# Kernel optimization log

Hardware: AMD Instinct MI355X
Metric: run time of the kernel (lower is better)

Reference implementation:

```python
import jax, jax.numpy as jnp
import numpy as np

NUM_EXPERTS = 8
TOP_K = 2


def setup_inputs() -> dict:
    key = jax.random.key(0)
    ks = jax.random.split(key, 5)
    B, T, D, H, E = 8, 4096, 512, 1536, NUM_EXPERTS
    scale = 0.02
    x = jax.random.normal(ks[0], (B, T, D), dtype=jnp.float32)
    gate_w = jax.random.normal(ks[1], (E, D), dtype=jnp.float32) * scale
    w1 = jax.random.normal(ks[2], (E, H, D), dtype=jnp.float32) * scale
    w3 = jax.random.normal(ks[3], (E, H, D), dtype=jnp.float32) * scale
    w2 = jax.random.normal(ks[4], (E, D, H), dtype=jnp.float32) * scale
    return {"x": x, "gate_w": gate_w, "w1": w1, "w3": w3, "w2": w2}


def reference(x, gate_w, w1, w3, w2):
    B, T, D = x.shape
    E = gate_w.shape[0]
    xf = x.reshape(-1, D)                      # [N, D], N = B*T
    N = xf.shape[0]
    gate_logits = xf @ gate_w.T                # [N, E]
    weights, indices = jax.lax.top_k(gate_logits, TOP_K)   # [N, K]
    weights = jax.nn.softmax(weights, axis=-1)
    # combine[n, e] = sum_k weights[n, k] * (indices[n, k] == e)
    combine = jnp.zeros((N, E), dtype=xf.dtype).at[
        jnp.arange(N)[:, None], indices].add(weights)       # [N, E]
    out = jnp.zeros_like(xf)
    for e in range(E):  # small fixed expert count
        h = jax.nn.silu(xf @ w1[e].T) * (xf @ w3[e].T)      # [N, H]
        y = h @ w2[e].T                                     # [N, D]
        out = out + combine[:, e:e + 1] * y
    return out.reshape(B, T, D)
```

## Files before the change

kernel.cpp:

```cpp
#include <hip/hip_runtime.h>


#define N_TOK 32768
#define DIM   512
#define HID   1536
#define NE    8
#define MTS   256

typedef __attribute__((ext_vector_type(8))) short  short8;
typedef __attribute__((ext_vector_type(4))) float  floatx4;

#define MFMA(a,b,c) __builtin_amdgcn_mfma_f32_16x16x32_bf16(a,b,c,0,0,0)

__device__ __forceinline__ unsigned short f2bf(float f) {
  unsigned int u = __float_as_uint(f);
  u += 0x7fffu + ((u >> 16) & 1u);
  return (unsigned short)(u >> 16);
}
__device__ __forceinline__ unsigned pk2(float a, float b) {
  return (unsigned)f2bf(a) | ((unsigned)f2bf(b) << 16);
}
__device__ __forceinline__ void gl_lds16(const unsigned short* g, unsigned short* l) {
  __builtin_amdgcn_global_load_lds(
      (const __attribute__((address_space(1))) unsigned int*)g,
      (__attribute__((address_space(3))) unsigned int*)l, 16, 0, 0);
}

__global__ void __launch_bounds__(256) cvt_kernel(const float* __restrict__ src,
                                                  unsigned short* __restrict__ dst,
                                                  int n4) {
  int i = blockIdx.x * 256 + threadIdx.x;
  if (i >= n4) return;
  float4 v = ((const float4*)src)[i];
  uint2 o; o.x = pk2(v.x, v.y); o.y = pk2(v.z, v.w);
  ((uint2*)dst)[i] = o;
}

__global__ void __launch_bounds__(256) gate1_kernel(const float* __restrict__ x,
                                                    const float* __restrict__ gw,
                                                    unsigned short* __restrict__ xb,
                                                    unsigned* __restrict__ eidx,
                                                    float* __restrict__ wts) {
  int lane = threadIdx.x & 63;
  int wave = threadIdx.x >> 6;
  int t = blockIdx.x * 4 + wave;

  const float4* xp = (const float4*)(x + (size_t)t * DIM + lane * 8);
  float4 x0 = xp[0], x1 = xp[1];

  uint4 o; o.x = pk2(x0.x, x0.y); o.y = pk2(x0.z, x0.w);
  o.z = pk2(x1.x, x1.y); o.w = pk2(x1.z, x1.w);
  *(uint4*)(xb + (size_t)t * DIM + lane * 8) = o;

  double p[NE];
#pragma unroll
  for (int e = 0; e < NE; ++e) {
    const float4* gp = (const float4*)(gw + e * DIM + lane * 8);
    float4 g0 = gp[0], g1 = gp[1];
    p[e] = (double)x0.x * g0.x + (double)x0.y * g0.y + (double)x0.z * g0.z + (double)x0.w * g0.w
         + (double)x1.x * g1.x + (double)x1.y * g1.y + (double)x1.z * g1.z + (double)x1.w * g1.w;
  }
#pragma unroll
  for (int m = 1; m < 64; m <<= 1) {
#pragma unroll
    for (int e = 0; e < NE; ++e) p[e] += __shfl_xor(p[e], m);
  }
  if (lane == 0) {
    double m1 = -1e300, m2 = -1e300; int i1 = 0, i2 = 0;
#pragma unroll
    for (int e = 0; e < NE; ++e) {
      double v = p[e];
      if (v > m1) { m2 = m1; i2 = i1; m1 = v; i1 = e; }
      else if (v > m2) { m2 = v; i2 = e; }
    }
    float e2 = __expf((float)(m2 - m1));
    float wa = 1.f / (1.f + e2);
    eidx[t] = (unsigned)i1 | ((unsigned)i2 << 8);
    wts[t]  = wa;
  }
}

__global__ void __launch_bounds__(256) gate2_kernel(const unsigned* __restrict__ eidx,
                                                    const float* __restrict__ wts,
                                                    int* __restrict__ tokl,
                                                    float* __restrict__ wgtl,
                                                    int* __restrict__ cnt) {
  __shared__ unsigned hist[NE];
  __shared__ unsigned basep[NE];
  int tid = threadIdx.x;
  if (tid < NE) hist[tid] = 0;
  __syncthreads();
  int t0 = blockIdx.x * 1024;
  unsigned pk[4]; float wv[4];
#pragma unroll
  for (int i = 0; i < 4; ++i) {
    int t = t0 + tid + i * 256;
    pk[i] = eidx[t]; wv[i] = wts[t];
    atomicAdd(&hist[pk[i] & 0xff], 1u);
    atomicAdd(&hist[(pk[i] >> 8) & 0xff], 1u);
  }
  __syncthreads();
  if (tid < NE) {
    basep[tid] = (unsigned)atomicAdd(&cnt[tid], (int)hist[tid]);
    hist[tid] = 0;
  }
  __syncthreads();
#pragma unroll
  for (int i = 0; i < 4; ++i) {
    int t = t0 + tid + i * 256;
    int e1 = pk[i] & 0xff, e2 = (pk[i] >> 8) & 0xff;
    unsigned p1 = basep[e1] + atomicAdd(&hist[e1], 1u);
    tokl[e1 * N_TOK + p1] = t; wgtl[e1 * N_TOK + p1] = wv[i];
    unsigned p2 = basep[e2] + atomicAdd(&hist[e2], 1u);
    tokl[e2 * N_TOK + p2] = t; wgtl[e2 * N_TOK + p2] = 1.f - wv[i];
  }
}

__global__ void __launch_bounds__(256, 4) ffn1_kernel(
    const unsigned short* __restrict__ xb,
    const unsigned short* __restrict__ w1b,
    const unsigned short* __restrict__ w3b,
    const int* __restrict__ tokl, const float* __restrict__ wgtl,
    const int* __restrict__ cnt,
    unsigned short* __restrict__ Hs,
    int h0base, int P, int NT) {
  int e  = blockIdx.x & 7;
  int t  = blockIdx.x >> 3;
  int nt = t % NT, mt = t / NT;
  int ne = cnt[e];
  int m0 = mt * 128;
  if (m0 >= ne) return;
  int offs = 0;
#pragma unroll
  for (int i = 0; i < NE; ++i) offs += (i < e) ? cnt[i] : 0;

  __shared__ __align__(16) unsigned short As[128 * 64];
  __shared__ __align__(16) unsigned short Bs[128 * 64];
  __shared__ float wgs[128];

  int tid = threadIdx.x, w = tid >> 6, lane = tid & 63;
  int quad = lane >> 4, l16 = lane & 15;
  int wm = w >> 1, wn = w & 1;

  if (tid < 128) {
    int r = m0 + tid;
    wgs[tid] = (r < ne) ? wgtl[e * N_TOK + r] : 0.f;
  }

  int rl = lane >> 3, cc = (lane & 7) ^ rl;
  const unsigned short* pa[4];
#pragma unroll
  for (int i = 0; i < 4; ++i) {
    int r = m0 + 32 * w + 8 * i + rl;
    int tok = tokl[e * N_TOK + (r < ne ? r : m0)];
    pa[i] = xb + (size_t)tok * DIM + cc * 8;
  }
  const unsigned short* wsrc = (w < 2) ? w1b : w3b;
  const unsigned short* pb0 =
      wsrc + ((size_t)e * HID + h0base + nt * 64 + ((32 * w) & 63) + rl) * DIM + cc * 8;

  floatx4 u[4][2], v[4][2];
#pragma unroll
  for (int i = 0; i < 4; ++i)
#pragma unroll
    for (int j = 0; j < 2; ++j) { u[i][j] = (floatx4){0,0,0,0}; v[i][j] = (floatx4){0,0,0,0}; }

  for (int k0 = 0; k0 < DIM; k0 += 64) {
#pragma unroll
    for (int i = 0; i < 4; ++i) {
      gl_lds16(pa[i], &As[(32 * w + 8 * i) * 64]);
      gl_lds16(pb0 + (size_t)i * 8 * DIM, &Bs[(32 * w + 8 * i) * 64]);
      pa[i] += 64;
    }
    pb0 += 64;
    __syncthreads();
#pragma unroll
    for (int kk = 0; kk < 2; ++kk) {
      int s = ((4 * kk + quad) ^ (l16 & 7)) * 8;
      short8 a[4], b1[2], b3[2];
#pragma unroll
      for (int i = 0; i < 4; ++i)
        a[i] = *(const short8*)&As[(wm * 64 + i * 16 + l16) * 64 + s];
#pragma unroll
      for (int j = 0; j < 2; ++j) {
        b1[j] = *(const short8*)&Bs[(wn * 32 + j * 16 + l16) * 64 + s];
        b3[j] = *(const short8*)&Bs[(64 + wn * 32 + j * 16 + l16) * 64 + s];
      }
#pragma unroll
      for (int i = 0; i < 4; ++i)
#pragma unroll
        for (int j = 0; j < 2; ++j) {
          u[i][j] = MFMA(a[i], b1[j], u[i][j]);
          v[i][j] = MFMA(a[i], b3[j], v[i][j]);
        }
    }
    __syncthreads();
  }

#pragma unroll
  for (int i = 0; i < 4; ++i)
#pragma unroll
    for (int j = 0; j < 2; ++j)
#pragma unroll
      for (int r = 0; r < 4; ++r) {
        int tr = wm * 64 + i * 16 + quad * 4 + r;
        int hc = wn * 32 + j * 16 + l16;
        float uu = u[i][j][r], vv = v[i][j][r];
        float h = (uu / (1.f + __expf(-uu))) * vv * wgs[tr];
        As[tr * 64 + hc] = f2bf(h);
      }
  __syncthreads();
  {
    int row = tid >> 1, half = tid & 1;
    if (m0 + row < ne) {
      const unsigned short* s = &As[row * 64 + half * 32];
      unsigned short* d = Hs + (size_t)(offs + m0 + row) * P + nt * 64 + half * 32;
#pragma unroll
      for (int j = 0; j < 4; ++j) *(uint4*)(d + j * 8) = *(const uint4*)(s + j * 8);
    }
  }
}

__global__ void __launch_bounds__(256, 4) ffn2_kernel(
    const unsigned short* __restrict__ Hs,
    const unsigned short* __restrict__ w2b,
    const int* __restrict__ tokl, const int* __restrict__ cnt,
    float* __restrict__ out, int h0base, int P) {
  int e  = blockIdx.x & 7;
  int t  = blockIdx.x >> 3;
  int nt = t & 3, mt = t >> 2;
  int ne = cnt[e];
  int m0 = mt * 128;
  if (m0 >= ne) return;
  int offs = 0;
#pragma unroll
  for (int i = 0; i < NE; ++i) offs += (i < e) ? cnt[i] : 0;

  __shared__ __align__(16) unsigned short As[128 * 64];
  __shared__ __align__(16) unsigned short Bs[128 * 64];
  __shared__ int toks[128];

  int tid = threadIdx.x, w = tid >> 6, lane = tid & 63;
  int quad = lane >> 4, l16 = lane & 15;
  int wm = w >> 1, wn = w & 1;
  if (tid < 128) { int r = m0 + tid; toks[tid] = tokl[e * N_TOK + (r < ne ? r : m0)]; }

  int rl = lane >> 3, cc = (lane & 7) ^ rl;
  int dbase = nt * 128;
  const unsigned short* pa0 = Hs + (size_t)(offs + m0 + 32 * w + rl) * P + cc * 8;
  const unsigned short* pb0 =
      w2b + ((size_t)e * DIM + dbase + 32 * w + rl) * HID + h0base + cc * 8;

  floatx4 acc[4][4];
#pragma unroll
  for (int i = 0; i < 4; ++i)
#pragma unroll
    for (int j = 0; j < 4; ++j) acc[i][j] = (floatx4){0,0,0,0};

  for (int k0 = 0; k0 < P; k0 += 64) {
#pragma unroll
    for (int i = 0; i < 4; ++i) {
      gl_lds16(pa0 + (size_t)i * 8 * P,   &As[(32 * w + 8 * i) * 64]);
      gl_lds16(pb0 + (size_t)i * 8 * HID, &Bs[(32 * w + 8 * i) * 64]);
    }
    pa0 += 64; pb0 += 64;
    __syncthreads();
#pragma unroll
    for (int kk = 0; kk < 2; ++kk) {
      int s = ((4 * kk + quad) ^ (l16 & 7)) * 8;
      short8 a[4], b[4];
#pragma unroll
      for (int i = 0; i < 4; ++i) {
        a[i] = *(const short8*)&As[(wm * 64 + i * 16 + l16) * 64 + s];
        b[i] = *(const short8*)&Bs[(wn * 64 + i * 16 + l16) * 64 + s];
      }
#pragma unroll
      for (int i = 0; i < 4; ++i)
#pragma unroll
        for (int j = 0; j < 4; ++j)
          acc[i][j] = MFMA(a[i], b[j], acc[i][j]);
    }
    __syncthreads();
  }

#pragma unroll
  for (int i = 0; i < 4; ++i)
#pragma unroll
    for (int j = 0; j < 4; ++j)
#pragma unroll
      for (int r = 0; r < 4; ++r) {
        int row = wm * 64 + i * 16 + quad * 4 + r;
        if (m0 + row < ne)
          atomicAdd(&out[(size_t)toks[row] * DIM + dbase + wn * 64 + j * 16 + l16],
                    acc[i][j][r]);
      }
}

extern "C" void kernel_launch(void* const* d_in, const int* in_sizes, int n_in,
                              void* d_out, int out_size, void* d_ws, size_t ws_size,
                              hipStream_t stream) {
  const float* x  = (const float*)d_in[0];
  const float* gw = (const float*)d_in[1];
  const float* w1 = (const float*)d_in[2];
  const float* w3 = (const float*)d_in[3];
  const float* w2 = (const float*)d_in[4];
  float* out = (float*)d_out;

  const size_t NW = (size_t)NE * HID * DIM;
  char* p = (char*)d_ws;
  unsigned short* w1b = (unsigned short*)p;  p += NW * 2;
  unsigned short* w3b = (unsigned short*)p;  p += NW * 2;
  unsigned short* w2b = (unsigned short*)p;  p += NW * 2;
  unsigned short* xb  = (unsigned short*)p;  p += (size_t)N_TOK * DIM * 2;
  int*      tokl = (int*)p;       p += (size_t)NE * N_TOK * 4;
  float*    wgtl = (float*)p;     p += (size_t)NE * N_TOK * 4;
  unsigned* eidx = (unsigned*)p;  p += (size_t)N_TOK * 4;
  float*    wts  = (float*)p;     p += (size_t)N_TOK * 4;
  int*      cnt  = (int*)p;       p += 256;
  unsigned short* Hs = (unsigned short*)p;
  size_t fixed = (size_t)(p - (char*)d_ws);
  if (ws_size < fixed) return;
  size_t avail = ws_size - fixed;

  const int cands[5] = {1536, 768, 512, 384, 256};
  int P = 0;
  for (int i = 0; i < 5; ++i)
    if ((size_t)(2 * N_TOK + 128) * cands[i] * 2 <= avail) { P = cands[i]; break; }
  if (!P) return;

  hipMemsetAsync(d_out, 0, (size_t)N_TOK * DIM * sizeof(float), stream);
  hipMemsetAsync(cnt, 0, NE * sizeof(int), stream);

  int n4 = (int)(NW / 4);
  cvt_kernel<<<n4 / 256, 256, 0, stream>>>(w1, w1b, n4);
  cvt_kernel<<<n4 / 256, 256, 0, stream>>>(w3, w3b, n4);
  cvt_kernel<<<n4 / 256, 256, 0, stream>>>(w2, w2b, n4);

  gate1_kernel<<<N_TOK / 4, 256, 0, stream>>>(x, gw, xb, eidx, wts);
  gate2_kernel<<<N_TOK / 1024, 256, 0, stream>>>(eidx, wts, tokl, wgtl, cnt);

  for (int h0 = 0; h0 < HID; h0 += P) {
    int NT = P / 64;
    ffn1_kernel<<<8 * MTS * NT, 256, 0, stream>>>(xb, w1b, w3b, tokl, wgtl, cnt, Hs, h0, P, NT);
    ffn2_kernel<<<8 * MTS * 4, 256, 0, stream>>>(Hs, w2b, tokl, cnt, out, h0, P);
  }
}
```

Measured before the change: 730.7 us.

## Replace atomic scatter in FFN2 with plain stores into two output buffers

```diff
diff --git a/kernel.cpp b/kernel.cpp
--- a/kernel.cpp
+++ b/kernel.cpp
@@ -112,7 +112,7 @@
     unsigned p1 = basep[e1] + atomicAdd(&hist[e1], 1u);
     tokl[e1 * N_TOK + p1] = t; wgtl[e1 * N_TOK + p1] = wv[i];
     unsigned p2 = basep[e2] + atomicAdd(&hist[e2], 1u);
-    tokl[e2 * N_TOK + p2] = t; wgtl[e2 * N_TOK + p2] = 1.f - wv[i];
+    tokl[e2 * N_TOK + p2] = t | (int)0x80000000; wgtl[e2 * N_TOK + p2] = 1.f - wv[i];
   }
 }
 
@@ -152,7 +152,7 @@
 #pragma unroll
   for (int i = 0; i < 4; ++i) {
     int r = m0 + 32 * w + 8 * i + rl;
-    int tok = tokl[e * N_TOK + (r < ne ? r : m0)];
+    int tok = tokl[e * N_TOK + (r < ne ? r : m0)] & 0x7fffffff;
     pa[i] = xb + (size_t)tok * DIM + cc * 8;
   }
   const unsigned short* wsrc = (w < 2) ? w1b : w3b;
@@ -225,7 +225,8 @@
     const unsigned short* __restrict__ Hs,
     const unsigned short* __restrict__ w2b,
     const int* __restrict__ tokl, const int* __restrict__ cnt,
-    float* __restrict__ out, int h0base, int P) {
+    float* __restrict__ out, float* __restrict__ prt,
+    int h0base, int P, int first) {
   int e  = blockIdx.x & 7;
   int t  = blockIdx.x >> 3;
   int nt = t & 3, mt = t >> 2;
@@ -286,14 +287,31 @@
 #pragma unroll
   for (int i = 0; i < 4; ++i)
 #pragma unroll
-    for (int j = 0; j < 4; ++j)
-#pragma unroll
-      for (int r = 0; r < 4; ++r) {
-        int row = wm * 64 + i * 16 + quad * 4 + r;
-        if (m0 + row < ne)
-          atomicAdd(&out[(size_t)toks[row] * DIM + dbase + wn * 64 + j * 16 + l16],
-                    acc[i][j][r]);
+    for (int r = 0; r < 4; ++r) {
+      int row = wm * 64 + i * 16 + quad * 4 + r;
+      if (m0 + row >= ne) continue;
+      int tk = toks[row];
+      float* dst = ((tk < 0) ? prt : out)
+                   + (size_t)(tk & 0x7fffffff) * DIM + dbase + wn * 64 + l16;
+      if (first) {
+#pragma unroll
+        for (int j = 0; j < 4; ++j) dst[j * 16] = acc[i][j][r];
+      } else {
+#pragma unroll
+        for (int j = 0; j < 4; ++j) dst[j * 16] += acc[i][j][r];
       }
+    }
+}
+
+__global__ void __launch_bounds__(256) combine_kernel(float* __restrict__ out,
+                                                      const float* __restrict__ prt,
+                                                      int n4) {
+  for (int i = blockIdx.x * 256 + threadIdx.x; i < n4; i += gridDim.x * 256) {
+    float4 a = ((const float4*)out)[i];
+    float4 b = ((const float4*)prt)[i];
+    a.x += b.x; a.y += b.y; a.z += b.z; a.w += b.w;
+    ((float4*)out)[i] = a;
+  }
 }
 
 extern "C" void kernel_launch(void* const* d_in, const int* in_sizes, int n_in,
@@ -317,6 +335,7 @@
   unsigned* eidx = (unsigned*)p;  p += (size_t)N_TOK * 4;
   float*    wts  = (float*)p;     p += (size_t)N_TOK * 4;
   int*      cnt  = (int*)p;       p += 256;
+  float*    prt  = (float*)p;     p += (size_t)N_TOK * DIM * 4;
   unsigned short* Hs = (unsigned short*)p;
   size_t fixed = (size_t)(p - (char*)d_ws);
   if (ws_size < fixed) return;
@@ -328,7 +347,6 @@
     if ((size_t)(2 * N_TOK + 128) * cands[i] * 2 <= avail) { P = cands[i]; break; }
   if (!P) return;
 
-  hipMemsetAsync(d_out, 0, (size_t)N_TOK * DIM * sizeof(float), stream);
   hipMemsetAsync(cnt, 0, NE * sizeof(int), stream);
 
   int n4 = (int)(NW / 4);
@@ -339,9 +357,12 @@
   gate1_kernel<<<N_TOK / 4, 256, 0, stream>>>(x, gw, xb, eidx, wts);
   gate2_kernel<<<N_TOK / 1024, 256, 0, stream>>>(eidx, wts, tokl, wgtl, cnt);
 
+  int pass = 0;
   for (int h0 = 0; h0 < HID; h0 += P) {
     int NT = P / 64;
     ffn1_kernel<<<8 * MTS * NT, 256, 0, stream>>>(xb, w1b, w3b, tokl, wgtl, cnt, Hs, h0, P, NT);
-    ffn2_kernel<<<8 * MTS * 4, 256, 0, stream>>>(Hs, w2b, tokl, cnt, out, h0, P);
-  }
-}
+    ffn2_kernel<<<8 * MTS * 4, 256, 0, stream>>>(Hs, w2b, tokl, cnt, out, prt, h0, P, pass == 0);
+    ++pass;
+  }
+  combine_kernel<<<2048, 256, 0, stream>>>(out, prt, N_TOK * DIM / 4);
+}
```

After: 686.6 us. -6.0%, faster.
